# Performance work log

Hardware: AMD Instinct MI355X
Metric: run time of the kernel (lower is better)

The kernel has to match this reference:

```python
import jax, jax.numpy as jnp
import numpy as np

EPS = 1e-5
GROUPS = 8
NUM_HEADS = 8


def setup_inputs() -> dict:
    key = jax.random.key(0)
    ks = jax.random.split(key, 6)
    C = 512
    s = 1.0 / np.sqrt(C)
    return {
        "x": jax.random.normal(ks[0], (8, C, 32, 32), dtype=jnp.float32),
        "gn_w": jnp.ones((C,), jnp.float32),
        "gn_b": jnp.zeros((C,), jnp.float32),
        "wq": jax.random.normal(ks[1], (C, C), jnp.float32) * s,
        "bq": jnp.zeros((C,), jnp.float32),
        "wk": jax.random.normal(ks[2], (C, C), jnp.float32) * s,
        "bk": jnp.zeros((C,), jnp.float32),
        "wv": jax.random.normal(ks[3], (C, C), jnp.float32) * s,
        "bv": jnp.zeros((C,), jnp.float32),
        "wp": jax.random.normal(ks[4], (C, C), jnp.float32) * s,
        "bp": jnp.zeros((C,), jnp.float32),
    }


def _group_norm(x, w, b):
    # x: [B, C, H, W]; normalize per group over (C//G, H, W)
    B, C, H, W = x.shape
    xg = x.reshape(B, GROUPS, -1)
    mean = xg.mean(axis=-1, keepdims=True)
    var = xg.var(axis=-1, keepdims=True)
    xn = ((xg - mean) * jax.lax.rsqrt(var + EPS)).reshape(B, C, H, W)
    return xn * w[None, :, None, None] + b[None, :, None, None]


def reference(x, gn_w, gn_b, wq, bq, wk, bk, wv, bv, wp, bp):
    B, C, H, W = x.shape
    n_heads = NUM_HEADS
    d = C // n_heads
    scale = 1.0 / np.sqrt(d)

    x_flat = x.reshape(B, C, H * W).transpose(0, 2, 1)       # [B, S, C]
    xn = _group_norm(x, gn_w, gn_b).reshape(B, C, H * W).transpose(0, 2, 1)

    # torch Linear: y = x @ W.T + b
    q = (xn @ wq.T + bq).reshape(B, H * W, n_heads, d)        # [B, S, h, d]
    k = (xn @ wk.T + bk).reshape(B, H * W, n_heads, d)
    v = (xn @ wv.T + bv).reshape(B, H * W, n_heads, d)

    attn = jnp.einsum("bnhd,bmhd->bhnm", q, k) * scale       # [B, h, S, S]
    attn = jax.nn.softmax(attn, axis=-1)
    out = jnp.einsum("bhnm,bmhd->bnhd", attn, v).reshape(B, H * W, C)
    out = out @ wp.T + bp
    out = out + x_flat
    return out.transpose(0, 2, 1).reshape(B, C, H, W)
```

## Files before the change

### kernel.cpp

```cpp
#include <hip/hip_runtime.h>
#include <stdint.h>

typedef unsigned short u16;
using bf16x8 = __attribute__((ext_vector_type(8))) short;
using f32x4  = __attribute__((ext_vector_type(4))) float;
using f32x16 = __attribute__((ext_vector_type(16))) float;
typedef unsigned int uv2 __attribute__((ext_vector_type(2)));

#define EPS_GN 1e-5f
#define SCL 0.18033688011112042f

__device__ __forceinline__ u16 f2bf(float f) {
  union { float f; uint32_t u; } x; x.f = f;
  uint32_t r = x.u + 0x7FFFu + ((x.u >> 16) & 1u);
  return (u16)(r >> 16);
}

__device__ __forceinline__ void gload_lds16(const void* g, void* l) {
  __builtin_amdgcn_global_load_lds(
      (const __attribute__((address_space(1))) unsigned int*)g,
      (__attribute__((address_space(3))) unsigned int*)l, 16, 0, 0);
}

__device__ __forceinline__ void fence_tile() {
  asm volatile("s_waitcnt vmcnt(0)" ::: "memory");
  __builtin_amdgcn_s_barrier();
  __builtin_amdgcn_sched_barrier(0);
}

__global__ __launch_bounds__(256) void prep(const float* __restrict__ x,
    float* __restrict__ part,
    const float4* __restrict__ wq, const float4* __restrict__ wk,
    const float4* __restrict__ wv, const float4* __restrict__ wp,
    const float* __restrict__ bq, const float* __restrict__ bk,
    const float* __restrict__ bv,
    u16* __restrict__ wqkv, u16* __restrict__ wpb, float* __restrict__ bqkv) {
  if (blockIdx.x < 512) {
    int bg = blockIdx.x >> 3, seg = blockIdx.x & 7;
    const float4* base = (const float4*)(x + (size_t)bg * 65536 + (size_t)seg * 8192);
    float s = 0.f, s2 = 0.f;
    for (int i = threadIdx.x; i < 2048; i += 256) {
      float4 v = base[i];
      s  += v.x + v.y + v.z + v.w;
      s2 += v.x*v.x + v.y*v.y + v.z*v.z + v.w*v.w;
    }
    for (int m = 1; m < 64; m <<= 1) { s += __shfl_xor(s, m); s2 += __shfl_xor(s2, m); }
    __shared__ float red[4][2];
    int wave = threadIdx.x >> 6;
    if ((threadIdx.x & 63) == 0) { red[wave][0] = s; red[wave][1] = s2; }
    __syncthreads();
    if (threadIdx.x == 0) {
      float a = 0.f, b = 0.f;
      for (int w = 0; w < 4; ++w) { a += red[w][0]; b += red[w][1]; }
      part[blockIdx.x * 2] = a; part[blockIdx.x * 2 + 1] = b;
    }
  } else {
    int i = (blockIdx.x - 512) * 256 + threadIdx.x;
    int seg = i >> 16, j = i & 65535;
    const float4* w = (seg == 0) ? wq : (seg == 1) ? wk : (seg == 2) ? wv : wp;
    u16* o = (seg < 3) ? (wqkv + seg * 262144) : wpb;
    float sc = (seg == 0) ? SCL : 1.f;
    float4 v = w[j];
    o[j*4+0] = f2bf(v.x*sc); o[j*4+1] = f2bf(v.y*sc);
    o[j*4+2] = f2bf(v.z*sc); o[j*4+3] = f2bf(v.w*sc);
    if (i < 1536) bqkv[i] = (i < 512) ? bq[i]*SCL : (i < 1024) ? bk[i-512] : bv[i-1024];
  }
}

__global__ __launch_bounds__(256) void gn_apply(const float* __restrict__ x,
    const float* __restrict__ part, const float* __restrict__ w,
    const float* __restrict__ bb, u16* __restrict__ xn) {
  __shared__ float t[32][33];
  int s0 = blockIdx.x * 32, c0 = blockIdx.y * 32, b = blockIdx.z;
  int g = c0 >> 6;
  float s = 0.f, s2 = 0.f;
  for (int q = 0; q < 8; ++q) {
    s  += part[((b*8+g)*8 + q)*2];
    s2 += part[((b*8+g)*8 + q)*2 + 1];
  }
  float mean = s * (1.f/65536.f);
  float rstd = rsqrtf(s2 * (1.f/65536.f) - mean*mean + EPS_GN);
  for (int i = 0; i < 4; ++i) {
    int c = c0 + threadIdx.y + i * 8;
    float v = x[((size_t)b*512 + c)*1024 + s0 + threadIdx.x];
    t[threadIdx.y + i*8][threadIdx.x] = (v - mean) * rstd * w[c] + bb[c];
  }
  __syncthreads();
  for (int i = 0; i < 4; ++i) {
    int sdx = s0 + threadIdx.y + i * 8;
    xn[((size_t)b*1024 + sdx)*512 + c0 + threadIdx.x] = f2bf(t[threadIdx.x][threadIdx.y + i*8]);
  }
}

__global__ __launch_bounds__(256) void qkv_gemm(const u16* __restrict__ X,
    const u16* __restrict__ W, const float* __restrict__ bias,
    u16* __restrict__ qkb, u16* __restrict__ vTb) {
  __shared__ __align__(16) u16 As[2*128*64];
  __shared__ __align__(16) u16 Bs[2*128*64];
  const int K = 512;
  int m0 = (blockIdx.x & 63) * 128, n0 = (blockIdx.x >> 6) * 128;
  int t = threadIdx.x, lane = t & 63, wave = t >> 6;
  int wm = wave >> 1, wn = wave & 1;
  int lr = lane & 15, lg = lane >> 4;
  f32x4 acc[4][4] = {};

  auto stage = [&](int k0, int bufi) {
    u16* Ab = As + bufi * 8192;
    u16* Bb = Bs + bufi * 8192;
#pragma unroll
    for (int c = 0; c < 4; ++c) {
      int chunk = wave * 4 + c;
      int e = chunk * 512 + lane * 8;
      int r = e >> 6, col = e & 63;
      int scol = col ^ ((r & 7) << 3);
      gload_lds16(X + (size_t)(m0 + r) * K + k0 + scol, (char*)Ab + chunk * 1024);
      gload_lds16(W + (size_t)(n0 + r) * K + k0 + scol, (char*)Bb + chunk * 1024);
    }
  };

  stage(0, 0);
  fence_tile();
  int buf = 0;
  for (int k0 = 0; k0 < K; k0 += 64) {
    if (k0 + 64 < K) stage(k0 + 64, buf ^ 1);
    const char* Ab = (const char*)(As + buf * 8192);
    const char* Bb = (const char*)(Bs + buf * 8192);
    bf16x8 af[4][2], bfr[4][2];
#pragma unroll
    for (int i = 0; i < 4; ++i)
#pragma unroll
      for (int kk = 0; kk < 2; ++kk) {
        int ra = wm * 64 + i * 16 + lr;
        int ca = kk * 64 + lg * 16;
        af[i][kk]  = *(const bf16x8*)(Ab + ((ra * 128 + ca) ^ ((ra & 7) << 4)));
        int rb = wn * 64 + i * 16 + lr;
        bfr[i][kk] = *(const bf16x8*)(Bb + ((rb * 128 + ca) ^ ((rb & 7) << 4)));
      }
    __builtin_amdgcn_s_setprio(1);
#pragma unroll
    for (int kk = 0; kk < 2; ++kk)
#pragma unroll
      for (int i = 0; i < 4; ++i)
#pragma unroll
        for (int j = 0; j < 4; ++j)
          acc[i][j] = __builtin_amdgcn_mfma_f32_16x16x32_bf16(af[i][kk], bfr[j][kk], acc[i][j], 0, 0, 0);
    __builtin_amdgcn_s_setprio(0);
    fence_tile();
    buf ^= 1;
  }
  if (n0 < 1024) {
    for (int i = 0; i < 4; ++i)
      for (int j = 0; j < 4; ++j) {
        int col = n0 + wn * 64 + j * 16 + lr;
        float bv = bias[col];
        int rowb = m0 + wm * 64 + i * 16 + lg * 4;
        for (int r = 0; r < 4; ++r)
          qkb[(size_t)(rowb + r) * 1024 + col] = f2bf(acc[i][j][r] + bv);
      }
  } else {
    for (int i = 0; i < 4; ++i)
      for (int j = 0; j < 4; ++j) {
        int col = n0 + wn * 64 + j * 16 + lr;
        float bv = bias[col];
        int rowb = m0 + wm * 64 + i * 16 + lg * 4;
        unsigned p0, p1;
        float v0 = acc[i][j][0] + bv, v1 = acc[i][j][1] + bv;
        float v2 = acc[i][j][2] + bv, v3 = acc[i][j][3] + bv;
        asm("v_cvt_pk_bf16_f32 %0, %1, %2" : "=v"(p0) : "v"(v0), "v"(v1));
        asm("v_cvt_pk_bf16_f32 %0, %1, %2" : "=v"(p1) : "v"(v2), "v"(v3));
        uint2 pk; pk.x = p0; pk.y = p1;
        *(uint2*)(vTb + (size_t)(col - 1024) * 8192 + rowb) = pk;
      }
  }
}

__global__ __launch_bounds__(256) void proj_gemm(const u16* __restrict__ Wt,
    const u16* __restrict__ X, const float* __restrict__ bias,
    const float* __restrict__ resid, float* __restrict__ Out) {
  __shared__ __align__(16) u16 As[2*128*64];
  __shared__ __align__(16) u16 Bs[2*64*64];
  const int K = 512;
  int m0 = blockIdx.x * 64, n0 = blockIdx.y * 128;
  int t = threadIdx.x, lane = t & 63, wave = t >> 6;
  int wm = wave >> 1, wn = wave & 1;
  int lr = lane & 15, lg = lane >> 4;
  f32x4 acc[4][2] = {};

  auto stage = [&](int k0, int bufi) {
    u16* Ab = As + bufi * 8192;
    u16* Bb = Bs + bufi * 4096;
#pragma unroll
    for (int c = 0; c < 4; ++c) {
      int chunk = wave * 4 + c;
      int e = chunk * 512 + lane * 8;
      int r = e >> 6, col = e & 63;
      int scol = col ^ ((r & 7) << 3);
      gload_lds16(Wt + (size_t)(n0 + r) * K + k0 + scol, (char*)Ab + chunk * 1024);
    }
#pragma unroll
    for (int c = 0; c < 2; ++c) {
      int chunk = wave * 2 + c;
      int e = chunk * 512 + lane * 8;
      int r = e >> 6, col = e & 63;
      int scol = col ^ ((r & 7) << 3);
      gload_lds16(X + (size_t)(m0 + r) * K + k0 + scol, (char*)Bb + chunk * 1024);
    }
  };

  stage(0, 0);
  fence_tile();
  int buf = 0;
  for (int k0 = 0; k0 < K; k0 += 64) {
    if (k0 + 64 < K) stage(k0 + 64, buf ^ 1);
    const char* Ab = (const char*)(As + buf * 8192);
    const char* Bb = (const char*)(Bs + buf * 4096);
    bf16x8 af[4][2], bfr[2][2];
#pragma unroll
    for (int kk = 0; kk < 2; ++kk) {
      int ca = kk * 64 + lg * 16;
#pragma unroll
      for (int i = 0; i < 4; ++i) {
        int ra = wm * 64 + i * 16 + lr;
        af[i][kk] = *(const bf16x8*)(Ab + ((ra * 128 + ca) ^ ((ra & 7) << 4)));
      }
#pragma unroll
      for (int j = 0; j < 2; ++j) {
        int rb = wn * 32 + j * 16 + lr;
        bfr[j][kk] = *(const bf16x8*)(Bb + ((rb * 128 + ca) ^ ((rb & 7) << 4)));
      }
    }
    __builtin_amdgcn_s_setprio(1);
#pragma unroll
    for (int kk = 0; kk < 2; ++kk)
#pragma unroll
      for (int i = 0; i < 4; ++i)
#pragma unroll
        for (int j = 0; j < 2; ++j)
          acc[i][j] = __builtin_amdgcn_mfma_f32_16x16x32_bf16(af[i][kk], bfr[j][kk], acc[i][j], 0, 0, 0);
    __builtin_amdgcn_s_setprio(0);
    fence_tile();
    buf ^= 1;
  }
  for (int i = 0; i < 4; ++i)
    for (int j = 0; j < 2; ++j) {
      int mcol = m0 + wn * 32 + j * 16 + lr;
      for (int r = 0; r < 4; ++r) {
        int nrow = n0 + wm * 64 + i * 16 + lg * 4 + r;
        float v = acc[i][j][r] + bias[nrow];
        size_t b = (size_t)(mcol >> 10); int s = mcol & 1023;
        size_t addr = (b * 512 + nrow) * 1024 + s;
        Out[addr] = v + resid[addr];
      }
    }
}

__global__ __launch_bounds__(512, 4) void attn_fwd(const u16* __restrict__ qk,
    const u16* __restrict__ vT, u16* __restrict__ o) {
  __shared__ __align__(16) u16 smem[32768];
  int bh = blockIdx.x, qb = blockIdx.y;
  int b = bh >> 3, h = bh & 7;
  int t = threadIdx.x, lane = t & 63, wave = t >> 6;
  int half = wave >> 2, wq4 = wave & 3;
  int lq = lane & 31, hi = lane >> 5;
  int qrow0 = qb * 128 + wq4 * 32;
  const u16* qp = qk + (size_t)(b * 1024 + qrow0 + lq) * 1024 + h * 64 + hi * 8;
  bf16x8 qf[4];
#pragma unroll
  for (int s = 0; s < 4; ++s) qf[s] = *(const bf16x8*)(qp + s * 16);
  float li = 0.f;
  f32x16 ot[2] = {};
  int kvbase = half * 512;

  auto stage = [&](int ti, int bufi) {
    u16* Kb = smem + (half * 2 + bufi) * 8192;
    u16* Vb = Kb + 4096;
    int kv = kvbase + ti * 64;
#pragma unroll
    for (int c = 0; c < 2; ++c) {
      int chunk = wq4 * 2 + c;
      int e = chunk * 512 + lane * 8;
      int r = e >> 6, col = e & 63;
      int scol = col ^ ((r & 7) << 3);
      gload_lds16(qk + (size_t)(b * 1024 + kv + r) * 1024 + 512 + h * 64 + scol,
                  (char*)Kb + chunk * 1024);
      gload_lds16(vT + (size_t)(h * 64 + r) * 8192 + b * 1024 + kv + scol,
                  (char*)Vb + chunk * 1024);
    }
  };

  stage(0, 0);
  fence_tile();
  int buf = 0;
  for (int ti = 0; ti < 8; ++ti) {
    if (ti < 7) stage(ti + 1, buf ^ 1);
    const char* Kb = (const char*)(smem + (half * 2 + buf) * 8192);
    const char* Vb = Kb + 8192;
    f32x16 st[2];
#pragma unroll
    for (int n2 = 0; n2 < 2; ++n2) {
      int rk = n2 * 32 + lq;
      f32x16 z = {};
      __builtin_amdgcn_s_setprio(1);
#pragma unroll
      for (int s = 0; s < 4; ++s) {
        bf16x8 kf = *(const bf16x8*)(Kb + ((rk * 128 + s * 32 + hi * 16) ^ ((rk & 7) << 4)));
        z = __builtin_amdgcn_mfma_f32_32x32x16_bf16(kf, qf[s], z, 0, 0, 0);
      }
      __builtin_amdgcn_s_setprio(0);
      st[n2] = z;
    }
    float sm[16];
#pragma unroll
    for (int r = 0; r < 16; ++r) {
      float e0 = __builtin_amdgcn_exp2f(st[0][r]);
      float e1 = __builtin_amdgcn_exp2f(st[1][r]);
      st[0][r] = e0; st[1][r] = e1;
      sm[r] = e0 + e1;
    }
#pragma unroll
    for (int s = 8; s > 0; s >>= 1)
#pragma unroll
      for (int r = 0; r < s; ++r) sm[r] += sm[r + s];
    li += sm[0] + __shfl_xor(sm[0], 32);
#pragma unroll
    for (int n2 = 0; n2 < 2; ++n2) {
#pragma unroll
      for (int c = 0; c < 2; ++c) {
        int cg = n2 * 2 + c;
        unsigned W0, W1, W2, W3;
        asm("v_cvt_pk_bf16_f32 %0, %1, %2" : "=v"(W0) : "v"(st[n2][8*c+0]), "v"(st[n2][8*c+1]));
        asm("v_cvt_pk_bf16_f32 %0, %1, %2" : "=v"(W1) : "v"(st[n2][8*c+2]), "v"(st[n2][8*c+3]));
        asm("v_cvt_pk_bf16_f32 %0, %1, %2" : "=v"(W2) : "v"(st[n2][8*c+4]), "v"(st[n2][8*c+5]));
        asm("v_cvt_pk_bf16_f32 %0, %1, %2" : "=v"(W3) : "v"(st[n2][8*c+6]), "v"(st[n2][8*c+7]));
        uv2 r02 = __builtin_amdgcn_permlane32_swap(W0, W2, false, false);
        uv2 r13 = __builtin_amdgcn_permlane32_swap(W1, W3, false, false);
        union { unsigned u[4]; bf16x8 v; } fr;
        fr.u[0] = r02[0]; fr.u[1] = r13[0]; fr.u[2] = r02[1]; fr.u[3] = r13[1];
        __builtin_amdgcn_s_setprio(1);
#pragma unroll
        for (int dt = 0; dt < 2; ++dt) {
          int rv = dt * 32 + lq;
          bf16x8 vf = *(const bf16x8*)(Vb + ((rv * 128 + cg * 32 + hi * 16) ^ ((rv & 7) << 4)));
          ot[dt] = __builtin_amdgcn_mfma_f32_32x32x16_bf16(vf, fr.v, ot[dt], 0, 0, 0);
        }
        __builtin_amdgcn_s_setprio(0);
      }
    }
    fence_tile();
    buf ^= 1;
  }
  float* cbuf = (float*)smem;
  float* wreg = cbuf + wq4 * 2176;
  if (half == 0) {
#pragma unroll
    for (int dt = 0; dt < 2; ++dt)
#pragma unroll
      for (int r = 0; r < 16; ++r)
        wreg[(dt * 16 + r) * 64 + lane] = ot[dt][r];
    wreg[2048 + lane] = li;
  }
  __syncthreads();
  if (half == 1) {
    float inv = 1.f / (wreg[2048 + lane] + li);
    u16* wb = smem + 18432 + wq4 * 2048;
#pragma unroll
    for (int dt = 0; dt < 2; ++dt)
#pragma unroll
      for (int g = 0; g < 4; ++g) {
        float v0 = (wreg[(dt*16 + 4*g+0)*64 + lane] + ot[dt][4*g+0]) * inv;
        float v1 = (wreg[(dt*16 + 4*g+1)*64 + lane] + ot[dt][4*g+1]) * inv;
        float v2 = (wreg[(dt*16 + 4*g+2)*64 + lane] + ot[dt][4*g+2]) * inv;
        float v3 = (wreg[(dt*16 + 4*g+3)*64 + lane] + ot[dt][4*g+3]) * inv;
        unsigned p0, p1;
        asm("v_cvt_pk_bf16_f32 %0, %1, %2" : "=v"(p0) : "v"(v0), "v"(v1));
        asm("v_cvt_pk_bf16_f32 %0, %1, %2" : "=v"(p1) : "v"(v2), "v"(v3));
        int ch = dt * 8 + 2 * g + hi;
        int pos = ch ^ ((lq & 7) << 1);
        uint2 wv; wv.x = p0; wv.y = p1;
        *(uint2*)((char*)wb + lq * 128 + pos * 8) = wv;
      }
    int q2 = lane >> 1, j0 = lane & 1;
#pragma unroll
    for (int jj = 0; jj < 4; ++jj) {
      int j = j0 + jj * 2;
      uint4 val = *(const uint4*)((const char*)wb + q2 * 128 + ((j ^ (q2 & 7)) << 4));
      *(uint4*)(o + (size_t)(b * 1024 + qrow0 + q2) * 512 + h * 64 + j * 8) = val;
    }
  }
}

extern "C" void kernel_launch(void* const* d_in, const int* in_sizes, int n_in,
                              void* d_out, int out_size, void* d_ws, size_t ws_size,
                              hipStream_t stream) {
  const float* x    = (const float*)d_in[0];
  const float* gn_w = (const float*)d_in[1];
  const float* gn_b = (const float*)d_in[2];
  const float* wq   = (const float*)d_in[3];
  const float* bq   = (const float*)d_in[4];
  const float* wk   = (const float*)d_in[5];
  const float* bk   = (const float*)d_in[6];
  const float* wv   = (const float*)d_in[7];
  const float* bv   = (const float*)d_in[8];
  const float* wp   = (const float*)d_in[9];
  const float* bp   = (const float*)d_in[10];

  char* ws = (char*)d_ws;
  float* part  = (float*)ws;
  float* bqkv  = (float*)(ws + 4096);
  u16* wqkv = (u16*)(ws + 16384);
  u16* wpb  = (u16*)(ws + 1589248);
  u16* xn   = (u16*)(ws + 2113536);
  u16* qkb  = (u16*)(ws + 10502144);
  u16* vTb  = (u16*)(ws + 27279360);
  u16* attno = xn;

  prep<<<1536, 256, 0, stream>>>(x, part,
      (const float4*)wq, (const float4*)wk, (const float4*)wv, (const float4*)wp,
      bq, bk, bv, wqkv, wpb, bqkv);
  gn_apply<<<dim3(32, 16, 8), dim3(32, 8), 0, stream>>>(x, part, gn_w, gn_b, xn);
  qkv_gemm<<<768, 256, 0, stream>>>(xn, wqkv, bqkv, qkb, vTb);
  attn_fwd<<<dim3(64, 8), 512, 0, stream>>>(qkb, vTb, attno);
  proj_gemm<<<dim3(128, 4), 256, 0, stream>>>(wpb, attno, bp, x, (float*)d_out);
}
```

Baseline: 76.35 us.

## Store V in MFMA-fragment order and load it directly into registers

The QKV GEMM epilogue now writes V in a layout pre-permuted into per-lane MFMA operand fragments per (head, batch, 64-row tile). The attention kernel then loads each V fragment straight from global memory into registers instead of staging V through LDS, which halves the attention LDS footprint and removes the LDS reads for V. The trade-offs are scattered 8-byte writes in the GEMM epilogue and global-load latency in the attention loop that is only partly hidden behind the QK^T work. Each V tile is also re-read by every wave instead of being shared through LDS.

```diff
diff --git a/kernel.cpp b/kernel.cpp
--- a/kernel.cpp
+++ b/kernel.cpp
@@ -94,7 +94,7 @@
 
 __global__ __launch_bounds__(256) void qkv_gemm(const u16* __restrict__ X,
     const u16* __restrict__ W, const float* __restrict__ bias,
-    u16* __restrict__ qkb, u16* __restrict__ vTb) {
+    u16* __restrict__ qkb, u16* __restrict__ vP) {
   __shared__ __align__(16) u16 As[2*128*64];
   __shared__ __align__(16) u16 Bs[2*128*64];
   const int K = 512;
@@ -163,13 +163,21 @@
         int col = n0 + wn * 64 + j * 16 + lr;
         float bv = bias[col];
         int rowb = m0 + wm * 64 + i * 16 + lg * 4;
+        int colV = col - 1024;
+        int h  = colV >> 6, dl = colV & 63;
+        int dt = dl >> 5,  lqv = dl & 31;
+        int bb2 = rowb >> 10, s_in = rowb & 1023;
+        int tile = s_in >> 6, kvl = s_in & 63;
+        int cg = kvl >> 4, hiv = (kvl >> 3) & 1, j0 = kvl & 7;
+        int ii = dt * 4 + cg, lv = hiv * 32 + lqv;
+        size_t u16off = ((size_t)((h * 8 + bb2) * 16 + tile)) * 4096 + (ii * 64 + lv) * 8 + j0;
         unsigned p0, p1;
         float v0 = acc[i][j][0] + bv, v1 = acc[i][j][1] + bv;
         float v2 = acc[i][j][2] + bv, v3 = acc[i][j][3] + bv;
         asm("v_cvt_pk_bf16_f32 %0, %1, %2" : "=v"(p0) : "v"(v0), "v"(v1));
         asm("v_cvt_pk_bf16_f32 %0, %1, %2" : "=v"(p1) : "v"(v2), "v"(v3));
         uint2 pk; pk.x = p0; pk.y = p1;
-        *(uint2*)(vTb + (size_t)(col - 1024) * 8192 + rowb) = pk;
+        *(uint2*)(vP + u16off) = pk;
       }
   }
 }
@@ -255,8 +263,8 @@
 }
 
 __global__ __launch_bounds__(512, 4) void attn_fwd(const u16* __restrict__ qk,
-    const u16* __restrict__ vT, u16* __restrict__ o) {
-  __shared__ __align__(16) u16 smem[32768];
+    const u16* __restrict__ vP, u16* __restrict__ o) {
+  __shared__ __align__(16) u16 smem[26624];
   int bh = blockIdx.x, qb = blockIdx.y;
   int b = bh >> 3, h = bh & 7;
   int t = threadIdx.x, lane = t & 63, wave = t >> 6;
@@ -270,10 +278,10 @@
   float li = 0.f;
   f32x16 ot[2] = {};
   int kvbase = half * 512;
+  const u16* vb = vP + ((size_t)((h * 8 + b) * 16 + half * 8)) * 4096 + (size_t)lane * 8;
 
   auto stage = [&](int ti, int bufi) {
-    u16* Kb = smem + (half * 2 + bufi) * 8192;
-    u16* Vb = Kb + 4096;
+    u16* Kb = smem + (half * 2 + bufi) * 4096;
     int kv = kvbase + ti * 64;
 #pragma unroll
     for (int c = 0; c < 2; ++c) {
@@ -283,8 +291,6 @@
       int scol = col ^ ((r & 7) << 3);
       gload_lds16(qk + (size_t)(b * 1024 + kv + r) * 1024 + 512 + h * 64 + scol,
                   (char*)Kb + chunk * 1024);
-      gload_lds16(vT + (size_t)(h * 64 + r) * 8192 + b * 1024 + kv + scol,
-                  (char*)Vb + chunk * 1024);
     }
   };
 
@@ -292,9 +298,11 @@
   fence_tile();
   int buf = 0;
   for (int ti = 0; ti < 8; ++ti) {
+    bf16x8 vr[8];
+#pragma unroll
+    for (int i = 0; i < 8; ++i) vr[i] = *(const bf16x8*)(vb + ti * 4096 + i * 512);
     if (ti < 7) stage(ti + 1, buf ^ 1);
-    const char* Kb = (const char*)(smem + (half * 2 + buf) * 8192);
-    const char* Vb = Kb + 8192;
+    const char* Kb = (const char*)(smem + (half * 2 + buf) * 4096);
     f32x16 st[2];
 #pragma unroll
     for (int n2 = 0; n2 < 2; ++n2) {
@@ -338,11 +346,8 @@
         fr.u[0] = r02[0]; fr.u[1] = r13[0]; fr.u[2] = r02[1]; fr.u[3] = r13[1];
         __builtin_amdgcn_s_setprio(1);
 #pragma unroll
-        for (int dt = 0; dt < 2; ++dt) {
-          int rv = dt * 32 + lq;
-          bf16x8 vf = *(const bf16x8*)(Vb + ((rv * 128 + cg * 32 + hi * 16) ^ ((rv & 7) << 4)));
-          ot[dt] = __builtin_amdgcn_mfma_f32_32x32x16_bf16(vf, fr.v, ot[dt], 0, 0, 0);
-        }
+        for (int dt = 0; dt < 2; ++dt)
+          ot[dt] = __builtin_amdgcn_mfma_f32_32x32x16_bf16(vr[dt * 4 + cg], fr.v, ot[dt], 0, 0, 0);
         __builtin_amdgcn_s_setprio(0);
       }
     }
@@ -411,14 +416,14 @@
   u16* wpb  = (u16*)(ws + 1589248);
   u16* xn   = (u16*)(ws + 2113536);
   u16* qkb  = (u16*)(ws + 10502144);
-  u16* vTb  = (u16*)(ws + 27279360);
+  u16* vPb  = (u16*)(ws + 27279360);
   u16* attno = xn;
 
   prep<<<1536, 256, 0, stream>>>(x, part,
       (const float4*)wq, (const float4*)wk, (const float4*)wv, (const float4*)wp,
       bq, bk, bv, wqkv, wpb, bqkv);
   gn_apply<<<dim3(32, 16, 8), dim3(32, 8), 0, stream>>>(x, part, gn_w, gn_b, xn);
-  qkv_gemm<<<768, 256, 0, stream>>>(xn, wqkv, bqkv, qkb, vTb);
-  attn_fwd<<<dim3(64, 8), 512, 0, stream>>>(qkb, vTb, attno);
+  qkv_gemm<<<768, 256, 0, stream>>>(xn, wqkv, bqkv, qkb, vPb);
+  attn_fwd<<<dim3(64, 8), 512, 0, stream>>>(qkb, vPb, attno);
   proj_gemm<<<dim3(128, 4), 256, 0, stream>>>(wpb, attno, bp, x, (float*)d_out);
 }
```

Measured after the change: 98.48 us. +29.0%, slower.
